# Kernel optimization log

Measured on AMD Instinct MI355X. Metric: run time of the kernel, lower is better.

Reference implementation:

```python
import jax, jax.numpy as jnp
import numpy as np

B, I, H = 4096, 2048, 2048

def setup_inputs() -> dict:
    key = jax.random.key(0)
    ks = jax.random.split(key, 7)
    sk = (1.0 / H) ** 0.5
    return {
        "x": jax.random.normal(ks[0], (B, I), dtype=jnp.float32),
        "prev_state": jax.random.normal(ks[1], (B, H), dtype=jnp.float32),
        "c_state": jax.random.normal(ks[2], (B, H), dtype=jnp.float32),
        "W_fg": jax.random.uniform(ks[3], (H, H + I), jnp.float32, -sk, sk),
        "W_ig": jax.random.uniform(ks[4], (H, H + I), jnp.float32, -sk, sk),
        "W_og": jax.random.uniform(ks[5], (H, H + I), jnp.float32, -sk, sk),
        "W_ol": jax.random.uniform(ks[6], (H, H + I), jnp.float32, -sk, sk),
    }

def reference(x, prev_state, c_state, W_fg, W_ig, W_og, W_ol):
    # concat_hx: [B, H+I]
    concat_hx = jnp.concatenate([prev_state, x], axis=1)
    # Fuse the 4 gate GEMMs into one [B, H+I] x [H+I, 4H] matmul
    W_all = jnp.concatenate([W_fg, W_ig, W_og, W_ol], axis=0)  # [4H, H+I]
    gates = concat_hx @ W_all.T  # [B, 4H]
    ft, it, ct_t, ot = jnp.split(jax.nn.sigmoid(gates), 4, axis=1)
    # NOTE: original uses sigmoid (not tanh) for the candidate cell state ct_t
    ct = ft * c_state + it * ct_t
    ht = ot * jnp.tanh(ct)
    return ht
```

## Files before the change

### kernel.cpp

```cpp
#include <hip/hip_runtime.h>
#include <hip/hip_bf16.h>
#include <cstdint>
#include <cstddef>


typedef __bf16 nbf16;
typedef nbf16 bf16x8 __attribute__((ext_vector_type(8)));
typedef float f32x4 __attribute__((ext_vector_type(4)));

static constexpr int MDIM = 4096;
static constexpr int NDIM = 8192;
static constexpr int KDIM = 4096;
static constexpr int HDIM = 2048;
static constexpr int KB   = KDIM * 2;

#define VMW4  asm volatile("s_waitcnt vmcnt(4)" ::: "memory")
#define VMW0  asm volatile("s_waitcnt vmcnt(0)" ::: "memory")
#define LGKM0 asm volatile("s_waitcnt lgkmcnt(0)" ::: "memory")
#define BAR   __builtin_amdgcn_s_barrier()
#define SB0   __builtin_amdgcn_sched_barrier(0)
#define PRIO1 __builtin_amdgcn_s_setprio(1)
#define PRIO0 __builtin_amdgcn_s_setprio(0)

__device__ __forceinline__ void async16(void* lds, const void* g) {
    __builtin_amdgcn_global_load_lds(
        (const __attribute__((address_space(1))) void*)g,
        (__attribute__((address_space(3))) void*)lds,
        16, 0, 0);
}

__device__ __forceinline__ float fsig(float x) {
    return __builtin_amdgcn_rcpf(1.0f + __expf(-x));
}
__device__ __forceinline__ float ftanh(float x) {
    return 2.0f * __builtin_amdgcn_rcpf(1.0f + __expf(-2.0f * x)) - 1.0f;
}

__device__ __forceinline__ void stage_A(const char* Ab, int X, int t, char* slot,
                                        int wave, int r0, int cb) {
    const char* s = Ab + (size_t)(X * 64 + r0) * KB + t * 128 + cb;
    async16(slot + wave * 1024, s);
    async16(slot + (wave + 8) * 1024, s + (size_t)128 * KB);
}
__device__ __forceinline__ void stage_B(const char* Wb, int Y, int t, char* slot,
                                        int wave, int rB0, int cb) {
    const char* s = Wb + (size_t)(rB0 + Y * 32) * KB + t * 128 + cb;
    async16(slot + wave * 1024, s);
    async16(slot + (wave + 8) * 1024, s + (size_t)128 * KB);
}

__device__ __forceinline__ void read_A(bf16x8 (&d)[4][2], const char* hb,
                                       int ar, int kc0, int kc1) {
#pragma unroll
    for (int m = 0; m < 4; ++m) {
        d[m][0] = *(const bf16x8*)(hb + ar + m * 2048 + kc0);
        d[m][1] = *(const bf16x8*)(hb + ar + m * 2048 + kc1);
    }
}
__device__ __forceinline__ void read_B(bf16x8 (&d)[2][2], const char* hb,
                                       int br, int kc0, int kc1) {
#pragma unroll
    for (int j = 0; j < 2; ++j) {
        d[j][0] = *(const bf16x8*)(hb + br + j * 2048 + kc0);
        d[j][1] = *(const bf16x8*)(hb + br + j * 2048 + kc1);
    }
}
__device__ __forceinline__ void mfma16(f32x4 (&acc)[8][4], int mh, int Y,
                                       const bf16x8 (&a)[4][2],
                                       const bf16x8 (&b)[2][2]) {
#pragma unroll
    for (int m = 0; m < 4; ++m)
#pragma unroll
        for (int j = 0; j < 2; ++j) {
            acc[mh * 4 + m][Y * 2 + j] = __builtin_amdgcn_mfma_f32_16x16x32_bf16(
                a[m][0], b[j][0], acc[mh * 4 + m][Y * 2 + j], 0, 0, 0);
            acc[mh * 4 + m][Y * 2 + j] = __builtin_amdgcn_mfma_f32_16x16x32_bf16(
                a[m][1], b[j][1], acc[mh * 4 + m][Y * 2 + j], 0, 0, 0);
        }
}

__global__ __launch_bounds__(256) void k_concat_cast(
        const float* __restrict__ prev, const float* __restrict__ x,
        __hip_bfloat16* __restrict__ A) {
    const size_t total8 = (size_t)MDIM * KDIM / 8;
    const size_t stride = (size_t)gridDim.x * blockDim.x;
    for (size_t i = (size_t)blockIdx.x * blockDim.x + threadIdx.x; i < total8;
         i += stride) {
        size_t e = i * 8;
        size_t b = e >> 12;
        int k = (int)(e & (KDIM - 1));
        const float* src = (k < HDIM) ? (prev + b * HDIM + k)
                                      : (x + b * HDIM + (k - HDIM));
        float4 v0 = *(const float4*)src;
        float4 v1 = *(const float4*)(src + 4);
        union { __hip_bfloat16 h[8]; int4 q; } u;
        u.h[0] = __float2bfloat16(v0.x); u.h[1] = __float2bfloat16(v0.y);
        u.h[2] = __float2bfloat16(v0.z); u.h[3] = __float2bfloat16(v0.w);
        u.h[4] = __float2bfloat16(v1.x); u.h[5] = __float2bfloat16(v1.y);
        u.h[6] = __float2bfloat16(v1.z); u.h[7] = __float2bfloat16(v1.w);
        *(int4*)(A + e) = u.q;
    }
}

__global__ __launch_bounds__(256) void k_cast_w(
        const float* __restrict__ w0, const float* __restrict__ w1,
        const float* __restrict__ w2, const float* __restrict__ w3,
        __hip_bfloat16* __restrict__ W) {
    const size_t total8 = (size_t)NDIM * KDIM / 8;
    const size_t stride = (size_t)gridDim.x * blockDim.x;
    for (size_t i = (size_t)blockIdx.x * blockDim.x + threadIdx.x; i < total8;
         i += stride) {
        size_t e = i * 8;
        int n = (int)(e >> 12);
        int k = (int)(e & (KDIM - 1));
        int g = n & 3;
        size_t h = (size_t)(n >> 2);
        const float* src = (g == 0 ? w0 : g == 1 ? w1 : g == 2 ? w2 : w3)
                           + h * KDIM + k;
        float4 v0 = *(const float4*)src;
        float4 v1 = *(const float4*)(src + 4);
        union { __hip_bfloat16 h[8]; int4 q; } u;
        u.h[0] = __float2bfloat16(v0.x); u.h[1] = __float2bfloat16(v0.y);
        u.h[2] = __float2bfloat16(v0.z); u.h[3] = __float2bfloat16(v0.w);
        u.h[4] = __float2bfloat16(v1.x); u.h[5] = __float2bfloat16(v1.y);
        u.h[6] = __float2bfloat16(v1.z); u.h[7] = __float2bfloat16(v1.w);
        *(int4*)(W + e) = u.q;
    }
}

__global__ __launch_bounds__(512, 2) void k_gemm(
        const __hip_bfloat16* __restrict__ A, const __hip_bfloat16* __restrict__ W,
        const float* __restrict__ c, float* __restrict__ out) {
    __shared__ __align__(16) char lds[131072];

    const int bid = blockIdx.x;
    const int xcd = bid & 7, j = bid >> 3;
    const int mt = (xcd >> 2) * 8 + (j >> 3);
    const int nt = (xcd & 3) * 8 + (j & 7);
    const int brow = mt * 256, bcol = nt * 256;

    const int tid = threadIdx.x;
    const int wave = tid >> 6, lane = tid & 63;
    const int wr = wave >> 2, wc = wave & 3;

    const char* Ab = (const char*)A + (size_t)brow * KB;
    const char* Wb = (const char*)W + (size_t)bcol * KB;

    char* const Ah00 = lds;
    char* const Ah01 = lds + 16384;
    char* const Ah10 = lds + 32768;
    char* const Ah11 = lds + 49152;
    char* const Bh00 = lds + 65536;
    char* const Bh01 = lds + 81920;
    char* const Bh10 = lds + 98304;
    char* const Bh11 = lds + 114688;

    const int r0  = wave * 8 + (lane >> 3);
    const int rB0 = ((r0 >> 5) << 6) + (r0 & 31);
    const int cb  = (((lane & 7) ^ (lane >> 3)) << 4);
    const int kg  = lane >> 4;
    const int ar  = (wr * 64 + (lane & 15)) * 128;
    const int br  = (wc * 32 + (lane & 15)) * 128;
    const int kc0 = ((kg ^ (lane & 7)) << 4);
    const int kc1 = (((4 + kg) ^ (lane & 7)) << 4);

    f32x4 acc[8][4] = {};
    bf16x8 a0[4][2], a1[4][2], b0[2][2], b1[2][2];

    stage_B(Wb, 0, 0, Bh00, wave, rB0, cb);
    stage_A(Ab, 0, 0, Ah00, wave, r0, cb);
    stage_A(Ab, 1, 0, Ah01, wave, r0, cb);
    stage_B(Wb, 1, 0, Bh01, wave, rB0, cb);
    stage_B(Wb, 0, 1, Bh10, wave, rB0, cb);
    stage_A(Ab, 0, 1, Ah10, wave, r0, cb);
    stage_A(Ab, 1, 1, Ah11, wave, r0, cb);
    stage_B(Wb, 1, 1, Bh11, wave, rB0, cb);
    VMW4;
    SB0; BAR;
    read_A(a0, Ah00, ar, kc0, kc1);
    read_B(b0, Bh00, br, kc0, kc1);
    LGKM0;
    SB0; BAR;

    for (int i = 0; i < 32; ++i) {
        const int t2 = (2 * i + 2) & 63;
        const int t3 = (2 * i + 3) & 63;

        read_A(a1, Ah01, ar, kc0, kc1);
        stage_B(Wb, 0, t2, Bh00, wave, rB0, cb);
        SB0;
        PRIO1; mfma16(acc, 0, 0, a0, b0); PRIO0;
        LGKM0; SB0;
        read_B(b1, Bh01, br, kc0, kc1);
        stage_A(Ab, 0, t2, Ah00, wave, r0, cb);
        SB0;
        PRIO1; mfma16(acc, 1, 0, a1, b0); PRIO0;
        LGKM0; SB0; BAR;
        read_B(b0, Bh10, br, kc0, kc1);
        stage_A(Ab, 1, t2, Ah01, wave, r0, cb);
        SB0;
        PRIO1; mfma16(acc, 1, 1, a1, b1); PRIO0;
        LGKM0; SB0;
        read_A(a1, Ah10, ar, kc0, kc1);
        stage_B(Wb, 1, t2, Bh01, wave, rB0, cb);
        SB0;
        PRIO1; mfma16(acc, 0, 1, a0, b1); PRIO0;
        LGKM0; VMW4; SB0; BAR;
        read_A(a0, Ah11, ar, kc0, kc1);
        stage_B(Wb, 0, t3, Bh10, wave, rB0, cb);
        SB0;
        PRIO1; mfma16(acc, 0, 0, a1, b0); PRIO0;
        LGKM0; SB0;
        read_B(b1, Bh11, br, kc0, kc1);
        stage_A(Ab, 0, t3, Ah10, wave, r0, cb);
        SB0;
        PRIO1; mfma16(acc, 1, 0, a0, b0); PRIO0;
        LGKM0; SB0; BAR;
        read_B(b0, Bh00, br, kc0, kc1);
        stage_A(Ab, 1, t3, Ah11, wave, r0, cb);
        SB0;
        PRIO1; mfma16(acc, 1, 1, a0, b1); PRIO0;
        LGKM0; SB0;
        read_A(a0, Ah00, ar, kc0, kc1);
        stage_B(Wb, 1, t3, Bh11, wave, rB0, cb);
        SB0;
        PRIO1; mfma16(acc, 0, 1, a1, b1); PRIO0;
        LGKM0; VMW4; SB0; BAR;
    }

    VMW0; LGKM0;
    BAR;
    __hip_bfloat16* cl = (__hip_bfloat16*)lds;
    const int h0 = bcol >> 2;
    #pragma unroll
    for (int p = 0; p < 2; ++p) {
        if (p) BAR;
        if (wr == p) {
            const int rb = ((lane >> 4) << 2);
            const int cbase = wc * 64 + (lane & 15);
            #pragma unroll
            for (int mi = 0; mi < 8; ++mi)
                #pragma unroll
                for (int ni = 0; ni < 4; ++ni)
                    #pragma unroll
                    for (int q = 0; q < 4; ++q)
                        cl[(rb + mi * 16 + q) * 256 + (cbase + ni * 16)] =
                            __float2bfloat16(acc[mi][ni][q]);
        }
        BAR;
        #pragma unroll
        for (int rnd = 0; rnd < 4; ++rnd) {
            const int row = rnd * 32 + (tid >> 4);
            const int ccol = (tid & 15) * 16;
            union { int4 q[2]; __hip_bfloat16 h[16]; } v;
            v.q[0] = *(const int4*)&cl[row * 256 + ccol];
            v.q[1] = *(const int4*)&cl[row * 256 + ccol + 8];
            const size_t R = (size_t)(brow + p * 128 + row);
            const int hh = h0 + (tid & 15) * 4;
            float4 cc = *(const float4*)(c + R * HDIM + hh);
            float cs[4] = {cc.x, cc.y, cc.z, cc.w};
            float ht[4];
            #pragma unroll
            for (int u = 0; u < 4; ++u) {
                float ft  = fsig(__bfloat162float(v.h[4 * u + 0]));
                float it  = fsig(__bfloat162float(v.h[4 * u + 1]));
                float ctt = fsig(__bfloat162float(v.h[4 * u + 2]));
                float ot  = fsig(__bfloat162float(v.h[4 * u + 3]));
                float ct  = ft * cs[u] + it * ctt;
                ht[u] = ot * ftanh(ct);
            }
            float4 o = {ht[0], ht[1], ht[2], ht[3]};
            *(float4*)(out + R * HDIM + hh) = o;
        }
    }
}

extern "C" void kernel_launch(void* const* d_in, const int* in_sizes, int n_in,
                              void* d_out, int out_size, void* d_ws, size_t ws_size,
                              hipStream_t stream) {
    const float* x    = (const float*)d_in[0];
    const float* prev = (const float*)d_in[1];
    const float* cst  = (const float*)d_in[2];
    const float* wfg  = (const float*)d_in[3];
    const float* wig  = (const float*)d_in[4];
    const float* wog  = (const float*)d_in[5];
    const float* wol  = (const float*)d_in[6];
    float* out = (float*)d_out;

    char* ws = (char*)d_ws;
    __hip_bfloat16* Abf = (__hip_bfloat16*)(ws);
    __hip_bfloat16* Wbf = (__hip_bfloat16*)(ws + 33554432);

    k_concat_cast<<<2048, 256, 0, stream>>>(prev, x, Abf);
    k_cast_w<<<2048, 256, 0, stream>>>(wfg, wig, wog, wol, Wbf);
    k_gemm<<<512, 512, 0, stream>>>(Abf, Wbf, cst, out);
}
```

Before: 266.5 us.

## Pre-swizzle weights into MFMA fragment layout and load B directly to registers

The weight cast kernel now writes W in a fragment-major layout matching the MFMA B-operand lane pattern, so the GEMM loads B fragments straight from global memory into registers with coalesced 16-byte loads instead of staging through LDS. LDS use halves (only A is staged), and the vmcnt waits are reworked for the new mix of in-flight loads. This removes B LDS writes, reads and bank traffic and could allow more occupancy. In exchange, B global-load latency sits directly on the register path, relying on the one-step-ahead prefetch to hide it.

```diff
diff --git a/kernel.cpp b/kernel.cpp
--- a/kernel.cpp
+++ b/kernel.cpp
@@ -14,7 +14,8 @@
 static constexpr int HDIM = 2048;
 static constexpr int KB   = KDIM * 2;
 
-#define VMW4  asm volatile("s_waitcnt vmcnt(4)" ::: "memory")
+#define VMW12 asm volatile("s_waitcnt vmcnt(12)" ::: "memory")
+#define VMW8  asm volatile("s_waitcnt vmcnt(8)" ::: "memory")
 #define VMW0  asm volatile("s_waitcnt vmcnt(0)" ::: "memory")
 #define LGKM0 asm volatile("s_waitcnt lgkmcnt(0)" ::: "memory")
 #define BAR   __builtin_amdgcn_s_barrier()
@@ -42,12 +43,6 @@
     async16(slot + wave * 1024, s);
     async16(slot + (wave + 8) * 1024, s + (size_t)128 * KB);
 }
-__device__ __forceinline__ void stage_B(const char* Wb, int Y, int t, char* slot,
-                                        int wave, int rB0, int cb) {
-    const char* s = Wb + (size_t)(rB0 + Y * 32) * KB + t * 128 + cb;
-    async16(slot + wave * 1024, s);
-    async16(slot + (wave + 8) * 1024, s + (size_t)128 * KB);
-}
 
 __device__ __forceinline__ void read_A(bf16x8 (&d)[4][2], const char* hb,
                                        int ar, int kc0, int kc1) {
@@ -57,14 +52,14 @@
         d[m][1] = *(const bf16x8*)(hb + ar + m * 2048 + kc1);
     }
 }
-__device__ __forceinline__ void read_B(bf16x8 (&d)[2][2], const char* hb,
-                                       int br, int kc0, int kc1) {
-#pragma unroll
-    for (int j = 0; j < 2; ++j) {
-        d[j][0] = *(const bf16x8*)(hb + br + j * 2048 + kc0);
-        d[j][1] = *(const bf16x8*)(hb + br + j * 2048 + kc1);
-    }
-}
+
+#define LOADB(dst, bYbase, t_) {                                              \
+    const char* _p = WfB + (bYbase) + (size_t)(t_) * 2048;                    \
+    dst[0][0] = *(const bf16x8*)(_p);                                         \
+    dst[0][1] = *(const bf16x8*)(_p + 1024);                                  \
+    dst[1][0] = *(const bf16x8*)(_p + 131072);                                \
+    dst[1][1] = *(const bf16x8*)(_p + 131072 + 1024); }
+
 __device__ __forceinline__ void mfma16(f32x4 (&acc)[8][4], int mh, int Y,
                                        const bf16x8 (&a)[4][2],
                                        const bf16x8 (&b)[2][2]) {
@@ -105,33 +100,36 @@
 __global__ __launch_bounds__(256) void k_cast_w(
         const float* __restrict__ w0, const float* __restrict__ w1,
         const float* __restrict__ w2, const float* __restrict__ w3,
-        __hip_bfloat16* __restrict__ W) {
-    const size_t total8 = (size_t)NDIM * KDIM / 8;
+        __hip_bfloat16* __restrict__ Wf) {
+    const size_t total = (size_t)512 * 128 * 64;
     const size_t stride = (size_t)gridDim.x * blockDim.x;
-    for (size_t i = (size_t)blockIdx.x * blockDim.x + threadIdx.x; i < total8;
-         i += stride) {
-        size_t e = i * 8;
-        int n = (int)(e >> 12);
-        int k = (int)(e & (KDIM - 1));
+    for (size_t u = (size_t)blockIdx.x * blockDim.x + threadIdx.x; u < total;
+         u += stride) {
+        int lane = (int)(u & 63);
+        int ks   = (int)((u >> 6) & 127);
+        int n16  = (int)(u >> 13);
+        int r    = lane & 15, cch = lane >> 4;
+        int n = n16 * 16 + r;
         int g = n & 3;
         size_t h = (size_t)(n >> 2);
+        int k = ks * 32 + cch * 8;
         const float* src = (g == 0 ? w0 : g == 1 ? w1 : g == 2 ? w2 : w3)
                            + h * KDIM + k;
         float4 v0 = *(const float4*)src;
         float4 v1 = *(const float4*)(src + 4);
-        union { __hip_bfloat16 h[8]; int4 q; } u;
-        u.h[0] = __float2bfloat16(v0.x); u.h[1] = __float2bfloat16(v0.y);
-        u.h[2] = __float2bfloat16(v0.z); u.h[3] = __float2bfloat16(v0.w);
-        u.h[4] = __float2bfloat16(v1.x); u.h[5] = __float2bfloat16(v1.y);
-        u.h[6] = __float2bfloat16(v1.z); u.h[7] = __float2bfloat16(v1.w);
-        *(int4*)(W + e) = u.q;
+        union { __hip_bfloat16 hh[8]; int4 q; } uu;
+        uu.hh[0] = __float2bfloat16(v0.x); uu.hh[1] = __float2bfloat16(v0.y);
+        uu.hh[2] = __float2bfloat16(v0.z); uu.hh[3] = __float2bfloat16(v0.w);
+        uu.hh[4] = __float2bfloat16(v1.x); uu.hh[5] = __float2bfloat16(v1.y);
+        uu.hh[6] = __float2bfloat16(v1.z); uu.hh[7] = __float2bfloat16(v1.w);
+        *(int4*)((char*)Wf + u * 16) = uu.q;
     }
 }
 
 __global__ __launch_bounds__(512, 2) void k_gemm(
-        const __hip_bfloat16* __restrict__ A, const __hip_bfloat16* __restrict__ W,
+        const __hip_bfloat16* __restrict__ A, const __hip_bfloat16* __restrict__ Wf,
         const float* __restrict__ c, float* __restrict__ out) {
-    __shared__ __align__(16) char lds[131072];
+    __shared__ __align__(16) char lds[65536];
 
     const int bid = blockIdx.x;
     const int xcd = bid & 7, j = bid >> 3;
@@ -143,89 +141,85 @@
     const int wave = tid >> 6, lane = tid & 63;
     const int wr = wave >> 2, wc = wave & 3;
 
-    const char* Ab = (const char*)A + (size_t)brow * KB;
-    const char* Wb = (const char*)W + (size_t)bcol * KB;
+    const char* Ab  = (const char*)A + (size_t)brow * KB;
+    const char* WfB = (const char*)Wf;
 
     char* const Ah00 = lds;
     char* const Ah01 = lds + 16384;
     char* const Ah10 = lds + 32768;
     char* const Ah11 = lds + 49152;
-    char* const Bh00 = lds + 65536;
-    char* const Bh01 = lds + 81920;
-    char* const Bh10 = lds + 98304;
-    char* const Bh11 = lds + 114688;
 
     const int r0  = wave * 8 + (lane >> 3);
-    const int rB0 = ((r0 >> 5) << 6) + (r0 & 31);
     const int cb  = (((lane & 7) ^ (lane >> 3)) << 4);
     const int kg  = lane >> 4;
     const int ar  = (wr * 64 + (lane & 15)) * 128;
-    const int br  = (wc * 32 + (lane & 15)) * 128;
     const int kc0 = ((kg ^ (lane & 7)) << 4);
     const int kc1 = (((4 + kg) ^ (lane & 7)) << 4);
 
+    const size_t n16b = (size_t)(bcol >> 4) + wc * 4;
+    const size_t bY0 = n16b * 131072 + (size_t)lane * 16;
+    const size_t bY1 = (n16b + 2) * 131072 + (size_t)lane * 16;
+
     f32x4 acc[8][4] = {};
-    bf16x8 a0[4][2], a1[4][2], b0[2][2], b1[2][2];
-
-    stage_B(Wb, 0, 0, Bh00, wave, rB0, cb);
+    bf16x8 a0[4][2], a1[4][2], bv0[2][2], bv1[2][2];
+
     stage_A(Ab, 0, 0, Ah00, wave, r0, cb);
     stage_A(Ab, 1, 0, Ah01, wave, r0, cb);
-    stage_B(Wb, 1, 0, Bh01, wave, rB0, cb);
-    stage_B(Wb, 0, 1, Bh10, wave, rB0, cb);
     stage_A(Ab, 0, 1, Ah10, wave, r0, cb);
     stage_A(Ab, 1, 1, Ah11, wave, r0, cb);
-    stage_B(Wb, 1, 1, Bh11, wave, rB0, cb);
-    VMW4;
+    LOADB(bv0, bY0, 0);
+    VMW8;
     SB0; BAR;
     read_A(a0, Ah00, ar, kc0, kc1);
-    read_B(b0, Bh00, br, kc0, kc1);
     LGKM0;
     SB0; BAR;
 
     for (int i = 0; i < 32; ++i) {
+        const int ta = 2 * i;
+        const int tb = 2 * i + 1;
         const int t2 = (2 * i + 2) & 63;
         const int t3 = (2 * i + 3) & 63;
 
+        LOADB(bv1, bY1, ta);
+        SB0;
         read_A(a1, Ah01, ar, kc0, kc1);
-        stage_B(Wb, 0, t2, Bh00, wave, rB0, cb);
-        SB0;
-        PRIO1; mfma16(acc, 0, 0, a0, b0); PRIO0;
+        SB0;
+        PRIO1; mfma16(acc, 0, 0, a0, bv0); PRIO0;
         LGKM0; SB0;
-        read_B(b1, Bh01, br, kc0, kc1);
         stage_A(Ab, 0, t2, Ah00, wave, r0, cb);
         SB0;
-        PRIO1; mfma16(acc, 1, 0, a1, b0); PRIO0;
-        LGKM0; SB0; BAR;
-        read_B(b0, Bh10, br, kc0, kc1);
+        PRIO1; mfma16(acc, 1, 0, a1, bv0); PRIO0;
+        VMW12; SB0; BAR;
+        LOADB(bv0, bY0, tb);
+        SB0;
         stage_A(Ab, 1, t2, Ah01, wave, r0, cb);
         SB0;
-        PRIO1; mfma16(acc, 1, 1, a1, b1); PRIO0;
+        PRIO1; mfma16(acc, 1, 1, a1, bv1); PRIO0;
+        SB0;
+        read_A(a1, Ah10, ar, kc0, kc1);
+        SB0;
+        PRIO1; mfma16(acc, 0, 1, a0, bv1); PRIO0;
+        LGKM0; VMW12; SB0; BAR;
+        LOADB(bv1, bY1, tb);
+        SB0;
+        read_A(a0, Ah11, ar, kc0, kc1);
+        SB0;
+        PRIO1; mfma16(acc, 0, 0, a1, bv0); PRIO0;
         LGKM0; SB0;
-        read_A(a1, Ah10, ar, kc0, kc1);
-        stage_B(Wb, 1, t2, Bh01, wave, rB0, cb);
-        SB0;
-        PRIO1; mfma16(acc, 0, 1, a0, b1); PRIO0;
-        LGKM0; VMW4; SB0; BAR;
-        read_A(a0, Ah11, ar, kc0, kc1);
-        stage_B(Wb, 0, t3, Bh10, wave, rB0, cb);
-        SB0;
-        PRIO1; mfma16(acc, 0, 0, a1, b0); PRIO0;
-        LGKM0; SB0;
-        read_B(b1, Bh11, br, kc0, kc1);
         stage_A(Ab, 0, t3, Ah10, wave, r0, cb);
         SB0;
-        PRIO1; mfma16(acc, 1, 0, a0, b0); PRIO0;
-        LGKM0; SB0; BAR;
-        read_B(b0, Bh00, br, kc0, kc1);
+        PRIO1; mfma16(acc, 1, 0, a0, bv0); PRIO0;
+        VMW12; SB0; BAR;
+        LOADB(bv0, bY0, t2);
+        SB0;
         stage_A(Ab, 1, t3, Ah11, wave, r0, cb);
         SB0;
-        PRIO1; mfma16(acc, 1, 1, a0, b1); PRIO0;
-        LGKM0; SB0;
+        PRIO1; mfma16(acc, 1, 1, a0, bv1); PRIO0;
+        SB0;
         read_A(a0, Ah00, ar, kc0, kc1);
-        stage_B(Wb, 1, t3, Bh11, wave, rB0, cb);
-        SB0;
-        PRIO1; mfma16(acc, 0, 1, a1, b1); PRIO0;
-        LGKM0; VMW4; SB0; BAR;
+        SB0;
+        PRIO1; mfma16(acc, 0, 1, a1, bv1); PRIO0;
+        LGKM0; VMW12; SB0; BAR;
     }
 
     VMW0; LGKM0;
```

Result: slower. 279.4 us (+4.8%).
